# Kernel tuning notes

Hardware: AMD Instinct MI355X
Metric: run time of the kernel (lower is better)

## Reference

```python
import jax, jax.numpy as jnp
import numpy as np

B, CIN, COUT = 16, 32, 64
H = W = 64
K = 3                      # kernel side
GRID_SIZE, SPLINE_ORDER = 5, 3
P = K * K                  # in_features of each KANLinear
GR0, GR1 = -1.0, 1.0       # grid_range


def make_grid():
    # torch: grid = arange(-k, G+k+1)*h + grid_range[0], expanded to (in_features, G+2k+1)
    h = (GR1 - GR0) / GRID_SIZE
    g = jnp.arange(-SPLINE_ORDER, GRID_SIZE + SPLINE_ORDER + 1, dtype=jnp.float32) * h + GR0
    return jnp.broadcast_to(g, (P, g.shape[0]))


def b_splines(x, grid):
    # Cox-de Boor recursion. x: (..., P) -> bases: (..., P, GRID_SIZE+SPLINE_ORDER)
    xe = x[..., None]
    bases = ((xe >= grid[:, :-1]) & (xe < grid[:, 1:])).astype(x.dtype)
    for j in range(1, SPLINE_ORDER + 1):
        left = (xe - grid[:, : -(j + 1)]) / (grid[:, j:-1] - grid[:, : -(j + 1)])
        right = (grid[:, j + 1 :] - xe) / (grid[:, j + 1 :] - grid[:, 1:-j])
        bases = left * bases[..., :-1] + right * bases[..., 1:]
    return bases


def setup_inputs() -> dict:
    key = jax.random.key(0)
    k1, k2, k3, k4 = jax.random.split(key, 4)
    x = jax.random.normal(k1, (B, CIN, H, W), dtype=jnp.float32)
    base_weight = jax.random.normal(k2, (COUT, CIN, P), dtype=jnp.float32) * (1.0 / np.sqrt(P))
    spline_weight = jax.random.normal(k3, (COUT, CIN, P, GRID_SIZE + SPLINE_ORDER), dtype=jnp.float32) * 0.1
    spline_scaler = jax.random.normal(k4, (COUT, CIN, P), dtype=jnp.float32) * (1.0 / np.sqrt(P))
    return {"x": x, "base_weight": base_weight, "spline_weight": spline_weight, "spline_scaler": spline_scaler}


def reference(x, base_weight, spline_weight, spline_scaler):
    grid = make_grid()
    # im2col like torch.nn.Unfold: (B, CIN*P, Hout, Wout), channel-major feature order
    patches = jax.lax.conv_general_dilated_patches(x, (K, K), (1, 1), "VALID")
    _, _, Ho, Wo = patches.shape
    patches = patches.reshape(B, CIN, P, Ho * Wo).transpose(0, 1, 3, 2)  # (B, CIN, L, P)
    # base branch: SiLU(x) @ base_weight^T, summed over input channels per output channel
    base_out = jnp.einsum("bclp,ocp->bol", jax.nn.silu(patches), base_weight)
    # spline branch: B-spline bases contracted with scaled spline weights
    bases = b_splines(patches, grid)                       # (B, CIN, L, P, G+k)
    scaled_w = spline_weight * spline_scaler[..., None]    # (COUT, CIN, P, G+k)
    spline_out = jnp.einsum("bclpg,ocpg->bol", bases, scaled_w)
    return (base_out + spline_out).reshape(B, COUT, Ho, Wo)
```

## Files before the change

kernel.cpp:

```cpp
#include <hip/hip_runtime.h>


typedef short v8s __attribute__((ext_vector_type(8)));
typedef float v4f __attribute__((ext_vector_type(4)));

#define FSPL_OFF   0u
#define FSILU_OFF  33554688u
#define WPACK_OFF  37749248u

__device__ __forceinline__ unsigned short f2bf(float f) {
  unsigned int u = __float_as_uint(f);
  u += 0x7fffu + ((u >> 16) & 1u);
  return (unsigned short)(u >> 16);
}

__global__ __launch_bounds__(256) void k_spline(const float* __restrict__ x,
                                                unsigned char* __restrict__ ws) {
  int pix = blockIdx.x * 256 + threadIdx.x;
  float v = x[pix];
  float bb[11];
#pragma unroll
  for (int i = 0; i < 11; ++i) {
    float t0 = -2.2f + 0.4f * i;
    bb[i] = (v >= t0 && v < t0 + 0.4f) ? 1.0f : 0.0f;
  }
#pragma unroll
  for (int j = 1; j <= 3; ++j) {
    float rj = 1.0f / (0.4f * j);
#pragma unroll
    for (int i = 0; i + j < 11; ++i) {
      float ti = -2.2f + 0.4f * i;
      float lf = (v - ti) * rj;
      float rt = ((ti + 0.4f * (j + 1)) - v) * rj;
      bb[i] = lf * bb[i] + rt * bb[i + 1];
    }
  }
  uint4 o;
  o.x = (unsigned)f2bf(bb[0]) | ((unsigned)f2bf(bb[1]) << 16);
  o.y = (unsigned)f2bf(bb[2]) | ((unsigned)f2bf(bb[3]) << 16);
  o.z = (unsigned)f2bf(bb[4]) | ((unsigned)f2bf(bb[5]) << 16);
  o.w = (unsigned)f2bf(bb[6]) | ((unsigned)f2bf(bb[7]) << 16);
  *(uint4*)(ws + FSPL_OFF + (size_t)pix * 16) = o;
}

__global__ __launch_bounds__(256) void k_silu(const float* __restrict__ x,
                                              unsigned char* __restrict__ ws) {
  int bid = blockIdx.x;
  int b = bid >> 6, y = bid & 63;
  int t = threadIdx.x;
  int xx = t & 63, cg = t >> 6;
  unsigned short h[8];
#pragma unroll
  for (int k = 0; k < 8; ++k) {
    int c = cg * 8 + k;
    float v = x[(((size_t)(b * 32 + c) * 64 + y) * 64) + xx];
    float s = v / (1.0f + __expf(-v));
    h[k] = f2bf(s);
  }
  uint4 o;
  o.x = (unsigned)h[0] | ((unsigned)h[1] << 16);
  o.y = (unsigned)h[2] | ((unsigned)h[3] << 16);
  o.z = (unsigned)h[4] | ((unsigned)h[5] << 16);
  o.w = (unsigned)h[6] | ((unsigned)h[7] << 16);
  *(uint4*)(ws + FSILU_OFF + (size_t)(b * 4096 + y * 64 + xx) * 64 + cg * 16) = o;
}

__global__ __launch_bounds__(256) void k_wpack(const float* __restrict__ bw,
                                               const float* __restrict__ sw,
                                               const float* __restrict__ sc,
                                               unsigned char* __restrict__ ws) {
  int tid = blockIdx.x * 256 + threadIdx.x;
  if (tid >= 165888) return;
  int e = tid & 7, lane = (tid >> 3) & 63, ot = (tid >> 9) & 3, s = tid >> 11;
  int k = s * 32 + ((lane >> 4) << 3) + e;
  int o = (ot << 4) + (lane & 15);
  float val;
  if (k < 2304) {
    int chunk = k / 24, u = k - chunk * 24;
    int dj = u >> 3, g = u & 7;
    int c = chunk / 3, di = chunk - c * 3;
    int p = di * 3 + dj;
    val = sw[((size_t)(o * 32 + c) * 9 + p) * 8 + g] * sc[(size_t)(o * 32 + c) * 9 + p];
  } else {
    int k2 = k - 2304;
    int tp = k2 >> 5, cc = k2 & 31;
    val = bw[(size_t)(o * 32 + cc) * 9 + tp];
  }
  *(unsigned short*)(ws + WPACK_OFF + (size_t)tid * 2) = f2bf(val);
}

__device__ __forceinline__ void ld16(unsigned char* ldsp, const unsigned char* gp) {
  __builtin_amdgcn_global_load_lds(
      (const __attribute__((address_space(1))) unsigned int*)gp,
      (__attribute__((address_space(3))) unsigned int*)ldsp, 16, 0, 0);
}

__global__ __launch_bounds__(256) void k_gemm(const unsigned char* __restrict__ ws,
                                              float* __restrict__ out) {
  __shared__ __align__(16) unsigned char wlds[2][36864];
  __shared__ __align__(16) unsigned char flds[2][25088];

  const int blk = blockIdx.x;
  const int b = blk >> 4, ig = blk & 15;
  const int i0 = ig * 4;
  const int tid = threadIdx.x;
  const int wave = tid >> 6, lane = tid & 63;
  const int q = lane >> 4, ln = lane & 15;
  const int i = i0 + wave;

  auto stage = [&](int tn, int bi) {
#pragma unroll
    for (int it = 0; it < 15; ++it) {
      const int u = wave + it * 4;
      if (it < 9) {
        ld16(&wlds[bi][u * 1024],
             ws + WPACK_OFF + (size_t)tn * 36864 + (size_t)u * 1024 + lane * 16);
      } else if (tn < 8) {
        const int v = u - 36;
        const int cp = v / 6, r = v - cp * 6;
        ld16(&flds[bi][v * 1024],
             ws + FSPL_OFF +
                 ((size_t)((b * 32 + tn * 4 + cp) * 64 + i0 + r)) * 1024 + lane * 16);
      } else {
        const int v = u - 36;
        const int r = v >> 2, p4 = v & 3;
        ld16(&flds[bi][v * 1024],
             ws + FSILU_OFF + (size_t)(b * 64 + i0 + r) * 4096 +
                 (p4 * 16 + (lane >> 2)) * 64 + ((lane & 3) ^ ((lane >> 2) & 3)) * 16);
      }
    }
  };

  int foff[9];
#pragma unroll
  for (int sg = 0; sg < 9; ++sg) {
    int rid = 4 * sg + q;
    int ch = rid / 3, sub = rid - ch * 3;
    int cp = ch / 3, di = ch - cp * 3;
    foff[sg] = (cp * 6 + wave + di) * 1024 + (sub + ln) * 16;
  }

  v4f acc[4][4];
#pragma unroll
  for (int a = 0; a < 4; ++a)
#pragma unroll
    for (int c = 0; c < 4; ++c) acc[a][c] = (v4f){0.f, 0.f, 0.f, 0.f};

  stage(0, 0);
  __syncthreads();

#pragma unroll 1
  for (int t = 0; t < 8; ++t) {
    stage(t + 1, (t + 1) & 1);
    const unsigned char* wb_base = wlds[t & 1];
    const unsigned char* fb_base = flds[t & 1];
#pragma unroll
    for (int sg = 0; sg < 9; ++sg) {
      v8s wb[4], fb[4];
#pragma unroll
      for (int ot = 0; ot < 4; ++ot)
        wb[ot] = *(const v8s*)(wb_base + sg * 4096 + ot * 1024 + lane * 16);
#pragma unroll
      for (int pt = 0; pt < 4; ++pt)
        fb[pt] = *(const v8s*)(fb_base + foff[sg] + pt * 256);
#pragma unroll
      for (int ot = 0; ot < 4; ++ot)
#pragma unroll
        for (int pt = 0; pt < 4; ++pt)
          acc[ot][pt] = __builtin_amdgcn_mfma_f32_16x16x32_bf16(
              wb[ot], fb[pt], acc[ot][pt], 0, 0, 0);
    }
    __syncthreads();
  }

#pragma unroll
  for (int e = 0; e < 9; ++e) {
    const int di = e / 3, dj = e % 3;
    v8s wb[4], fb[4];
#pragma unroll
    for (int ot = 0; ot < 4; ++ot)
      wb[ot] = *(const v8s*)(&wlds[0][0] + e * 4096 + ot * 1024 + lane * 16);
    const int xb = dj + ln;
    const int sbase = (wave + di) * 4096 + xb * 64 + ((q ^ (xb & 3)) * 16);
#pragma unroll
    for (int pt = 0; pt < 4; ++pt)
      fb[pt] = *(const v8s*)(&flds[0][0] + sbase + pt * 1024);
#pragma unroll
    for (int ot = 0; ot < 4; ++ot)
#pragma unroll
      for (int pt = 0; pt < 4; ++pt)
        acc[ot][pt] = __builtin_amdgcn_mfma_f32_16x16x32_bf16(
            wb[ot], fb[pt], acc[ot][pt], 0, 0, 0);
  }

  if (i < 62) {
#pragma unroll
    for (int ot = 0; ot < 4; ++ot)
#pragma unroll
      for (int pt = 0; pt < 4; ++pt) {
        const int j = pt * 16 + ln;
        if (j < 62) {
#pragma unroll
          for (int r = 0; r < 4; ++r) {
            const int o = ot * 16 + q * 4 + r;
            out[(((size_t)b * 64 + o) * 62 + i) * 62 + j] = acc[ot][pt][r];
          }
        }
      }
  }
}

extern "C" void kernel_launch(void* const* d_in, const int* in_sizes, int n_in,
                              void* d_out, int out_size, void* d_ws, size_t ws_size,
                              hipStream_t stream) {
  const float* x  = (const float*)d_in[0];
  const float* bw = (const float*)d_in[1];
  const float* sw = (const float*)d_in[2];
  const float* sc = (const float*)d_in[3];
  unsigned char* ws = (unsigned char*)d_ws;
  float* out = (float*)d_out;

  hipLaunchKernelGGL(k_spline, dim3(8192), dim3(256), 0, stream, x, ws);
  hipLaunchKernelGGL(k_silu,   dim3(1024), dim3(256), 0, stream, x, ws);
  hipLaunchKernelGGL(k_wpack,  dim3(648),  dim3(256), 0, stream, bw, sw, sc, ws);
  hipLaunchKernelGGL(k_gemm,   dim3(256),  dim3(256), 0, stream, ws, out);
}
```

Before: 111.0 us.

## Split GEMM output channels across two waves per row with 512-thread blocks

Doubles the GEMM block to 8 waves. Each pair of waves shares an output row and splits the 64 output channels in half, so each wave holds 8 accumulators instead of 16. Staging loads are spread over 8 waves instead of 4. This is meant to raise latency hiding and MFMA issue parallelism, since the grid of only 256 blocks underfills the GPU. The cost is that feature fragments are loaded from LDS twice, once per wave of the pair, and each block synchronises more waves.

```diff
diff --git a/kernel.cpp b/kernel.cpp
--- a/kernel.cpp
+++ b/kernel.cpp
@@ -95,7 +95,7 @@
       (__attribute__((address_space(3))) unsigned int*)ldsp, 16, 0, 0);
 }
 
-__global__ __launch_bounds__(256) void k_gemm(const unsigned char* __restrict__ ws,
+__global__ __launch_bounds__(512) void k_gemm(const unsigned char* __restrict__ ws,
                                               float* __restrict__ out) {
   __shared__ __align__(16) unsigned char wlds[2][36864];
   __shared__ __align__(16) unsigned char flds[2][25088];
@@ -106,27 +106,30 @@
   const int tid = threadIdx.x;
   const int wave = tid >> 6, lane = tid & 63;
   const int q = lane >> 4, ln = lane & 15;
-  const int i = i0 + wave;
+  const int r = wave >> 1;
+  const int oh = wave & 1;
+  const int i = i0 + r;
 
   auto stage = [&](int tn, int bi) {
 #pragma unroll
-    for (int it = 0; it < 15; ++it) {
-      const int u = wave + it * 4;
-      if (it < 9) {
+    for (int it = 0; it < 8; ++it) {
+      const int u = wave + it * 8;
+      if (u < 36) {
         ld16(&wlds[bi][u * 1024],
              ws + WPACK_OFF + (size_t)tn * 36864 + (size_t)u * 1024 + lane * 16);
-      } else if (tn < 8) {
+      } else if (u < 60) {
         const int v = u - 36;
-        const int cp = v / 6, r = v - cp * 6;
-        ld16(&flds[bi][v * 1024],
-             ws + FSPL_OFF +
-                 ((size_t)((b * 32 + tn * 4 + cp) * 64 + i0 + r)) * 1024 + lane * 16);
-      } else {
-        const int v = u - 36;
-        const int r = v >> 2, p4 = v & 3;
-        ld16(&flds[bi][v * 1024],
-             ws + FSILU_OFF + (size_t)(b * 64 + i0 + r) * 4096 +
-                 (p4 * 16 + (lane >> 2)) * 64 + ((lane & 3) ^ ((lane >> 2) & 3)) * 16);
+        if (tn < 8) {
+          const int cp = v / 6, rr = v - cp * 6;
+          ld16(&flds[bi][v * 1024],
+               ws + FSPL_OFF +
+                   ((size_t)((b * 32 + tn * 4 + cp) * 64 + i0 + rr)) * 1024 + lane * 16);
+        } else {
+          const int rr = v >> 2, p4 = v & 3;
+          ld16(&flds[bi][v * 1024],
+               ws + FSILU_OFF + (size_t)(b * 64 + i0 + rr) * 4096 +
+                   (p4 * 16 + (lane >> 2)) * 64 + ((lane & 3) ^ ((lane >> 2) & 3)) * 16);
+        }
       }
     }
   };
@@ -137,12 +140,12 @@
     int rid = 4 * sg + q;
     int ch = rid / 3, sub = rid - ch * 3;
     int cp = ch / 3, di = ch - cp * 3;
-    foff[sg] = (cp * 6 + wave + di) * 1024 + (sub + ln) * 16;
-  }
-
-  v4f acc[4][4];
-#pragma unroll
-  for (int a = 0; a < 4; ++a)
+    foff[sg] = (cp * 6 + r + di) * 1024 + (sub + ln) * 16;
+  }
+
+  v4f acc[2][4];
+#pragma unroll
+  for (int a = 0; a < 2; ++a)
 #pragma unroll
     for (int c = 0; c < 4; ++c) acc[a][c] = (v4f){0.f, 0.f, 0.f, 0.f};
 
@@ -156,19 +159,19 @@
     const unsigned char* fb_base = flds[t & 1];
 #pragma unroll
     for (int sg = 0; sg < 9; ++sg) {
-      v8s wb[4], fb[4];
-#pragma unroll
-      for (int ot = 0; ot < 4; ++ot)
-        wb[ot] = *(const v8s*)(wb_base + sg * 4096 + ot * 1024 + lane * 16);
+      v8s wb[2], fb[4];
+#pragma unroll
+      for (int tt = 0; tt < 2; ++tt)
+        wb[tt] = *(const v8s*)(wb_base + sg * 4096 + (oh * 2 + tt) * 1024 + lane * 16);
 #pragma unroll
       for (int pt = 0; pt < 4; ++pt)
         fb[pt] = *(const v8s*)(fb_base + foff[sg] + pt * 256);
 #pragma unroll
-      for (int ot = 0; ot < 4; ++ot)
+      for (int tt = 0; tt < 2; ++tt)
 #pragma unroll
         for (int pt = 0; pt < 4; ++pt)
-          acc[ot][pt] = __builtin_amdgcn_mfma_f32_16x16x32_bf16(
-              wb[ot], fb[pt], acc[ot][pt], 0, 0, 0);
+          acc[tt][pt] = __builtin_amdgcn_mfma_f32_16x16x32_bf16(
+              wb[tt], fb[pt], acc[tt][pt], 0, 0, 0);
     }
     __syncthreads();
   }
@@ -176,34 +179,34 @@
 #pragma unroll
   for (int e = 0; e < 9; ++e) {
     const int di = e / 3, dj = e % 3;
-    v8s wb[4], fb[4];
-#pragma unroll
-    for (int ot = 0; ot < 4; ++ot)
-      wb[ot] = *(const v8s*)(&wlds[0][0] + e * 4096 + ot * 1024 + lane * 16);
+    v8s wb[2], fb[4];
+#pragma unroll
+    for (int tt = 0; tt < 2; ++tt)
+      wb[tt] = *(const v8s*)(&wlds[0][0] + e * 4096 + (oh * 2 + tt) * 1024 + lane * 16);
     const int xb = dj + ln;
-    const int sbase = (wave + di) * 4096 + xb * 64 + ((q ^ (xb & 3)) * 16);
+    const int sbase = (r + di) * 4096 + xb * 64 + ((q ^ (xb & 3)) * 16);
 #pragma unroll
     for (int pt = 0; pt < 4; ++pt)
       fb[pt] = *(const v8s*)(&flds[0][0] + sbase + pt * 1024);
 #pragma unroll
-    for (int ot = 0; ot < 4; ++ot)
+    for (int tt = 0; tt < 2; ++tt)
 #pragma unroll
       for (int pt = 0; pt < 4; ++pt)
-        acc[ot][pt] = __builtin_amdgcn_mfma_f32_16x16x32_bf16(
-            wb[ot], fb[pt], acc[ot][pt], 0, 0, 0);
+        acc[tt][pt] = __builtin_amdgcn_mfma_f32_16x16x32_bf16(
+            wb[tt], fb[pt], acc[tt][pt], 0, 0, 0);
   }
 
   if (i < 62) {
 #pragma unroll
-    for (int ot = 0; ot < 4; ++ot)
+    for (int tt = 0; tt < 2; ++tt)
 #pragma unroll
       for (int pt = 0; pt < 4; ++pt) {
         const int j = pt * 16 + ln;
         if (j < 62) {
 #pragma unroll
-          for (int r = 0; r < 4; ++r) {
-            const int o = ot * 16 + q * 4 + r;
-            out[(((size_t)b * 64 + o) * 62 + i) * 62 + j] = acc[ot][pt][r];
+          for (int rr = 0; rr < 4; ++rr) {
+            const int o = (oh * 2 + tt) * 16 + q * 4 + rr;
+            out[(((size_t)b * 64 + o) * 62 + i) * 62 + j] = acc[tt][pt][rr];
           }
         }
       }
@@ -223,5 +226,5 @@
   hipLaunchKernelGGL(k_spline, dim3(8192), dim3(256), 0, stream, x, ws);
   hipLaunchKernelGGL(k_silu,   dim3(1024), dim3(256), 0, stream, x, ws);
   hipLaunchKernelGGL(k_wpack,  dim3(648),  dim3(256), 0, stream, bw, sw, sc, ws);
-  hipLaunchKernelGGL(k_gemm,   dim3(256),  dim3(256), 0, stream, ws, out);
-}
+  hipLaunchKernelGGL(k_gemm,   dim3(256),  dim3(512), 0, stream, ws, out);
+}
```

Measured after the change: 105.6 us. -4.8%, faster.

## Split GEMM K dimension across two wave groups with LDS reduction

Applied to the files above, without the earlier changes.

Doubles the GEMM block to 512 threads and splits the reduction over input channels between two halves of the waves. Each half works on its own LDS buffer, and the partial sums are then combined through LDS before the store. Double-buffered prefetch overlap is replaced by a load-then-compute scheme separated by barriers. The aim is more waves per CU to hide latency with 256 blocks, at the cost of the lost load/compute overlap and an extra reduction step.

```diff
diff --git a/kernel.cpp b/kernel.cpp
--- a/kernel.cpp
+++ b/kernel.cpp
@@ -95,10 +95,10 @@
       (__attribute__((address_space(3))) unsigned int*)ldsp, 16, 0, 0);
 }
 
-__global__ __launch_bounds__(256) void k_gemm(const unsigned char* __restrict__ ws,
+__global__ __launch_bounds__(512) void k_gemm(const unsigned char* __restrict__ ws,
                                               float* __restrict__ out) {
-  __shared__ __align__(16) unsigned char wlds[2][36864];
-  __shared__ __align__(16) unsigned char flds[2][25088];
+  __shared__ __align__(16) unsigned char wl[2][36864];
+  __shared__ __align__(16) unsigned char fl[2][25088];
 
   const int blk = blockIdx.x;
   const int b = blk >> 4, ig = blk & 15;
@@ -106,27 +106,46 @@
   const int tid = threadIdx.x;
   const int wave = tid >> 6, lane = tid & 63;
   const int q = lane >> 4, ln = lane & 15;
-  const int i = i0 + wave;
-
-  auto stage = [&](int tn, int bi) {
+  const int kh = wave >> 2, r = wave & 3;
+  const int i = i0 + r;
+
+  auto stage = [&](int t) {
 #pragma unroll
     for (int it = 0; it < 15; ++it) {
-      const int u = wave + it * 4;
-      if (it < 9) {
-        ld16(&wlds[bi][u * 1024],
-             ws + WPACK_OFF + (size_t)tn * 36864 + (size_t)u * 1024 + lane * 16);
-      } else if (tn < 8) {
-        const int v = u - 36;
-        const int cp = v / 6, r = v - cp * 6;
-        ld16(&flds[bi][v * 1024],
-             ws + FSPL_OFF +
-                 ((size_t)((b * 32 + tn * 4 + cp) * 64 + i0 + r)) * 1024 + lane * 16);
+      const int u = wave + it * 8;
+      if (t < 4) {
+        if (u < 36) {
+          ld16(&wl[0][u * 1024],
+               ws + WPACK_OFF + (size_t)t * 36864 + (size_t)u * 1024 + lane * 16);
+        } else if (u < 72) {
+          const int v = u - 36;
+          ld16(&wl[1][v * 1024],
+               ws + WPACK_OFF + (size_t)(4 + t) * 36864 + (size_t)v * 1024 + lane * 16);
+        } else if (u < 96) {
+          const int v = u - 72;
+          const int cp = v / 6, rr = v - cp * 6;
+          const int y = min(i0 + rr, 63);
+          ld16(&fl[0][v * 1024],
+               ws + FSPL_OFF + ((size_t)((b * 32 + t * 4 + cp) * 64 + y)) * 1024 + lane * 16);
+        } else {
+          const int v = u - 96;
+          const int cp = v / 6, rr = v - cp * 6;
+          const int y = min(i0 + rr, 63);
+          ld16(&fl[1][v * 1024],
+               ws + FSPL_OFF + ((size_t)((b * 32 + 16 + t * 4 + cp) * 64 + y)) * 1024 + lane * 16);
+        }
       } else {
-        const int v = u - 36;
-        const int r = v >> 2, p4 = v & 3;
-        ld16(&flds[bi][v * 1024],
-             ws + FSILU_OFF + (size_t)(b * 64 + i0 + r) * 4096 +
-                 (p4 * 16 + (lane >> 2)) * 64 + ((lane & 3) ^ ((lane >> 2) & 3)) * 16);
+        if (u < 36) {
+          ld16(&wl[0][u * 1024],
+               ws + WPACK_OFF + (size_t)8 * 36864 + (size_t)u * 1024 + lane * 16);
+        } else if (u >= 72 && u < 96) {
+          const int v = u - 72;
+          const int rr = v >> 2, p4 = v & 3;
+          const int y = min(i0 + rr, 63);
+          ld16(&fl[0][v * 1024],
+               ws + FSILU_OFF + (size_t)(b * 64 + y) * 4096 +
+                   (p4 * 16 + (lane >> 2)) * 64 + ((lane & 3) ^ ((lane >> 2) & 3)) * 16);
+        }
       }
     }
   };
@@ -137,7 +156,7 @@
     int rid = 4 * sg + q;
     int ch = rid / 3, sub = rid - ch * 3;
     int cp = ch / 3, di = ch - cp * 3;
-    foff[sg] = (cp * 6 + wave + di) * 1024 + (sub + ln) * 16;
+    foff[sg] = (cp * 6 + r + di) * 1024 + (sub + ln) * 16;
   }
 
   v4f acc[4][4];
@@ -146,14 +165,13 @@
 #pragma unroll
     for (int c = 0; c < 4; ++c) acc[a][c] = (v4f){0.f, 0.f, 0.f, 0.f};
 
-  stage(0, 0);
+  stage(0);
   __syncthreads();
 
 #pragma unroll 1
-  for (int t = 0; t < 8; ++t) {
-    stage(t + 1, (t + 1) & 1);
-    const unsigned char* wb_base = wlds[t & 1];
-    const unsigned char* fb_base = flds[t & 1];
+  for (int t = 0; t < 4; ++t) {
+    const unsigned char* wb_base = wl[kh];
+    const unsigned char* fb_base = fl[kh];
 #pragma unroll
     for (int sg = 0; sg < 9; ++sg) {
       v8s wb[4], fb[4];
@@ -171,20 +189,22 @@
               wb[ot], fb[pt], acc[ot][pt], 0, 0, 0);
     }
     __syncthreads();
-  }
-
-#pragma unroll
-  for (int e = 0; e < 9; ++e) {
-    const int di = e / 3, dj = e % 3;
+    stage(t + 1);
+    __syncthreads();
+  }
+
+  const int p_lo = kh ? 5 : 0, p_hi = kh ? 9 : 5;
+  for (int p = p_lo; p < p_hi; ++p) {
+    const int di = p / 3, dj = p - di * 3;
     v8s wb[4], fb[4];
 #pragma unroll
     for (int ot = 0; ot < 4; ++ot)
-      wb[ot] = *(const v8s*)(&wlds[0][0] + e * 4096 + ot * 1024 + lane * 16);
+      wb[ot] = *(const v8s*)(&wl[0][0] + p * 4096 + ot * 1024 + lane * 16);
     const int xb = dj + ln;
-    const int sbase = (wave + di) * 4096 + xb * 64 + ((q ^ (xb & 3)) * 16);
+    const int sbase = (r + di) * 4096 + xb * 64 + ((q ^ (xb & 3)) * 16);
 #pragma unroll
     for (int pt = 0; pt < 4; ++pt)
-      fb[pt] = *(const v8s*)(&flds[0][0] + sbase + pt * 1024);
+      fb[pt] = *(const v8s*)(&fl[0][0] + sbase + pt * 1024);
 #pragma unroll
     for (int ot = 0; ot < 4; ++ot)
 #pragma unroll
@@ -193,20 +213,40 @@
             wb[ot], fb[pt], acc[ot][pt], 0, 0, 0);
   }
 
-  if (i < 62) {
-#pragma unroll
-    for (int ot = 0; ot < 4; ++ot)
-#pragma unroll
-      for (int pt = 0; pt < 4; ++pt) {
-        const int j = pt * 16 + ln;
-        if (j < 62) {
-#pragma unroll
-          for (int r = 0; r < 4; ++r) {
-            const int o = ot * 16 + q * 4 + r;
-            out[(((size_t)b * 64 + o) * 62 + i) * 62 + j] = acc[ot][pt][r];
+  __syncthreads();
+  float* red = (float*)&wl[0][0];
+  if (kh == 1) {
+    float* dst = red + r * 4096 + lane * 4;
+#pragma unroll
+    for (int ot = 0; ot < 4; ++ot)
+#pragma unroll
+      for (int pt = 0; pt < 4; ++pt)
+        *(v4f*)(dst + (ot * 4 + pt) * 256) = acc[ot][pt];
+  }
+  __syncthreads();
+  if (kh == 0) {
+    const float* srcp = red + r * 4096 + lane * 4;
+#pragma unroll
+    for (int ot = 0; ot < 4; ++ot)
+#pragma unroll
+      for (int pt = 0; pt < 4; ++pt)
+        acc[ot][pt] += *(const v4f*)(srcp + (ot * 4 + pt) * 256);
+
+    if (i < 62) {
+#pragma unroll
+      for (int ot = 0; ot < 4; ++ot)
+#pragma unroll
+        for (int pt = 0; pt < 4; ++pt) {
+          const int j = pt * 16 + ln;
+          if (j < 62) {
+#pragma unroll
+            for (int rr = 0; rr < 4; ++rr) {
+              const int o = ot * 16 + q * 4 + rr;
+              out[(((size_t)b * 64 + o) * 62 + i) * 62 + j] = acc[ot][pt][rr];
+            }
           }
         }
-      }
+    }
   }
 }
 
@@ -223,5 +263,5 @@
   hipLaunchKernelGGL(k_spline, dim3(8192), dim3(256), 0, stream, x, ws);
   hipLaunchKernelGGL(k_silu,   dim3(1024), dim3(256), 0, stream, x, ws);
   hipLaunchKernelGGL(k_wpack,  dim3(648),  dim3(256), 0, stream, bw, sw, sc, ws);
-  hipLaunchKernelGGL(k_gemm,   dim3(256),  dim3(256), 0, stream, ws, out);
-}
+  hipLaunchKernelGGL(k_gemm,   dim3(256),  dim3(512), 0, stream, ws, out);
+}
```

Result: faster. 108.4 us (-2.3%).
